# Kernel tuning notes

Measured on AMD Instinct MI355X. Metric: run time of the kernel, lower is better.

Reference implementation:

```python
import jax, jax.numpy as jnp
import numpy as np

N_NODES = 102400
N_EDGES = 1638400
N_REL = 8
D_IN = 256


def setup_inputs() -> dict:
    key = jax.random.key(0)
    ks = jax.random.split(key, 8)
    b_z = jax.random.normal(ks[0], (N_NODES, D_IN), dtype=jnp.float32)
    b_edge_index = jax.random.randint(ks[1], (2, N_EDGES), 0, N_NODES, dtype=jnp.int64)
    b_edge_weights = jax.random.uniform(ks[2], (N_EDGES,), dtype=jnp.float32)
    b_edge_types = jax.random.randint(ks[3], (N_EDGES,), 0, N_REL, dtype=jnp.int64)
    # Glorot-ish init scaled by fan-in
    W1 = jax.random.normal(ks[4], (N_REL, 256, 128), dtype=jnp.float32) / np.sqrt(256.0)
    W2 = jax.random.normal(ks[5], (N_REL, 128, 64), dtype=jnp.float32) / np.sqrt(128.0)
    W3 = jax.random.normal(ks[6], (N_REL, 64, 1), dtype=jnp.float32) / np.sqrt(64.0)
    return {
        "b_z": b_z,
        "b_edge_index": b_edge_index,
        "b_edge_weights": b_edge_weights,
        "b_edge_types": b_edge_types,
        "W1": W1, "bias1": jnp.zeros((128,), jnp.float32),
        "W2": W2, "bias2": jnp.zeros((64,), jnp.float32),
        "W3": W3, "bias3": jnp.zeros((1,), jnp.float32),
        "b_size": 512,
    }


def rgcn_conv(x, src, dst, etype, ew, W, b):
    """Relation-specific transform + weighted scatter-add (root_weight=False).

    x: [N, d_in], W: [R, d_in, d_out], b: [d_out]
    """
    n = x.shape[0]
    # Transform node features under every relation: [R, N, d_out]
    xw = jnp.einsum('nd,rdo->rno', x, W)
    # Per-edge message = W_{etype[e]} @ x[src[e]], scaled by edge weight
    msgs = xw[etype, src] * ew[:, None]          # [E, d_out]
    out = jax.ops.segment_sum(msgs, dst, num_segments=n)  # scatter-add at targets
    return out + b


def reference(b_z, b_edge_index, b_edge_weights, b_edge_types,
              W1, bias1, W2, bias2, W3, bias3, b_size):
    src, dst = b_edge_index[0], b_edge_index[1]
    h = rgcn_conv(b_z, src, dst, b_edge_types, b_edge_weights, W1, bias1)
    h = jax.nn.relu(h)
    h = rgcn_conv(h, src, dst, b_edge_types, b_edge_weights, W2, bias2)
    h = jax.nn.relu(h)
    h = rgcn_conv(h, src, dst, b_edge_types, b_edge_weights, W3, bias3)  # [N, 1]
    x_hat = h.reshape(b_size, -1)
    return x_hat
```

## Files before the change

kernel.cpp:

```cpp
#include <hip/hip_runtime.h>
#include <hip/hip_bf16.h>
#include <hip/hip_fp16.h>
#include <cstdint>

#define N_NODES 102400
#define N_EDGES 1638400
#define N_REL   8
#define D0      256
#define D1      128
#define D2      64

#define WIN     256
#define NBIN    (N_NODES / WIN)
#define CHA     8192
#define NBLKA   (N_EDGES / CHA)

typedef __attribute__((ext_vector_type(8))) short          s16x8;
typedef __attribute__((ext_vector_type(8))) unsigned short u16x8;
typedef __attribute__((ext_vector_type(4))) float          f32x4;

__device__ __forceinline__ unsigned short f2bf(float f) {
    unsigned u = __float_as_uint(f);
    u += 0x7fffu + ((u >> 16) & 1u);
    return (unsigned short)(u >> 16);
}
__device__ __forceinline__ float h2f_bits(unsigned short u) {
    __half_raw r; r.x = u;
    return __half2float(__half(r));
}

__global__ __launch_bounds__(256) void fill0_k(int* __restrict__ p, int total) {
    int i = blockIdx.x * 256 + threadIdx.x;
    if (i < total) p[i] = 0;
}

__global__ __launch_bounds__(256) void countA_k(const int* __restrict__ dst,
                                                int* __restrict__ bincnt) {
    __shared__ int h[NBIN];
    const int t  = threadIdx.x;
    const int e0 = blockIdx.x * CHA;
    for (int i = t; i < NBIN; i += 256) h[i] = 0;
    __syncthreads();
#pragma unroll
    for (int i = 0; i < CHA / 256; ++i) {
        int e = e0 + t + i * 256;
        if (e < N_EDGES) atomicAdd(&h[dst[e] >> 8], 1);
    }
    __syncthreads();
    for (int i = t; i < NBIN; i += 256) {
        int c = h[i];
        if (c) atomicAdd(&bincnt[i], c);
    }
}

__device__ __forceinline__ int block_scan_excl_512(int v, int* sA, int* sB, int t) {
    sA[t] = v;
    __syncthreads();
    int* s = sA; int* d = sB;
    for (int o = 1; o < 512; o <<= 1) {
        int x = s[t];
        if (t >= o) x += s[t - o];
        d[t] = x;
        __syncthreads();
        int* tmp = s; s = d; d = tmp;
    }
    return s[t] - v;
}

__global__ __launch_bounds__(512) void scanB_k(const int* __restrict__ bincnt,
                                               int* __restrict__ binbase,
                                               int* __restrict__ bincur) {
    __shared__ int sA[512], sB[512];
    const int t = threadIdx.x;
    int v = (t < NBIN) ? bincnt[t] : 0;
    int excl = block_scan_excl_512(v, sA, sB, t);
    if (t < NBIN) { binbase[t] = excl; bincur[t] = excl; }
    if (t == 0) binbase[NBIN] = N_EDGES;
}

__global__ __launch_bounds__(256) void scatterA_k(const int* __restrict__ src,
                                                  const int* __restrict__ dst,
                                                  const float* __restrict__ ew,
                                                  const int* __restrict__ et,
                                                  int* __restrict__ bincur,
                                                  uint2* __restrict__ temp) {
    __shared__ int h[NBIN];
    const int t  = threadIdx.x;
    const int e0 = blockIdx.x * CHA;
    for (int i = t; i < NBIN; i += 256) h[i] = 0;
    __syncthreads();
#pragma unroll
    for (int i = 0; i < CHA / 256; ++i) {
        int e = e0 + t + i * 256;
        if (e < N_EDGES) atomicAdd(&h[dst[e] >> 8], 1);
    }
    __syncthreads();
    for (int i = t; i < NBIN; i += 256) {
        int c = h[i];
        h[i] = c ? atomicAdd(&bincur[i], c) : 0;
    }
    __syncthreads();
#pragma unroll
    for (int i = 0; i < CHA / 256; ++i) {
        int e = e0 + t + i * 256;
        if (e < N_EDGES) {
            int d   = dst[e];
            int bin = d >> 8;
            unsigned hb = (unsigned)(__half_raw(__float2half(ew[e])).x);
            unsigned g  = (unsigned)(et[e] * N_NODES + src[e]);
            int pos = atomicAdd(&h[bin], 1);
            temp[pos] = make_uint2(g, (hb << 8) | (unsigned)(d & 255));
        }
    }
}

__global__ __launch_bounds__(512) void passB_k(const uint2* __restrict__ temp,
                                               const int* __restrict__ binbase,
                                               int* __restrict__ off,
                                               unsigned* __restrict__ eg,
                                               unsigned short* __restrict__ ewh) {
    __shared__ int hist[WIN];
    __shared__ int sA[512], sB[512];
    const int b    = blockIdx.x;
    const int t    = threadIdx.x;
    const int beg  = binbase[b], end = binbase[b + 1];
    const int key0 = b * WIN;
    if (t < WIN) hist[t] = 0;
    __syncthreads();
    for (int j = beg + t; j < end; j += 512)
        atomicAdd(&hist[temp[j].y & 255], 1);
    __syncthreads();
    int v = (t < WIN) ? hist[t] : 0;
    int excl = block_scan_excl_512(v, sA, sB, t) + beg;
    if (t < WIN) {
        off[key0 + t] = excl;
        hist[t] = excl;
    }
    __syncthreads();
    for (int j = beg + t; j < end; j += 512) {
        uint2 e = temp[j];
        int pos = atomicAdd(&hist[e.y & 255], 1);
        eg[pos]  = e.x;
        ewh[pos] = (unsigned short)(e.y >> 8);
    }
    if (b == 0 && t == 0) off[N_NODES] = N_EDGES;
}

__global__ __launch_bounds__(256) void cvt_wT_k(const float* __restrict__ in,
                                                unsigned short* __restrict__ out,
                                                int K, int Nn, int total) {
    int o = blockIdx.x * 256 + threadIdx.x;
    if (o < total) {
        int kn = K * Nn;
        int r = o / kn, rem = o % kn;
        int n = rem / K, k = rem % K;
        out[o] = f2bf(in[r * kn + k * Nn + n]);
    }
}

template<int DIN, int DOUT, bool AF32>
__global__ __launch_bounds__(256) void mfma_gemm_b(const void* __restrict__ Av,
                                                   const unsigned short* __restrict__ Bt0,
                                                   __half* __restrict__ C0) {
    constexpr int BM  = 128;
    constexpr int BK  = 64;
    constexpr int BN  = DOUT;
    constexpr int LDK = BK + 8;
    constexpr int FM  = (BM / 2) / 16;
    constexpr int FN  = (BN / 2) / 16;

    __shared__ __align__(16) unsigned short As[BM][LDK];
    __shared__ __align__(16) unsigned short Bs[BN][LDK];

    const unsigned short* Bt = Bt0 + (size_t)blockIdx.y * DIN * DOUT;
    __half*               C  = C0  + (size_t)blockIdx.y * N_NODES * DOUT;

    const int tid  = threadIdx.x;
    const int wave = tid >> 6;
    const int lane = tid & 63;
    const int lr   = lane & 15;
    const int kq   = lane >> 4;
    const int wm   = (wave >> 1) * (BM / 2);
    const int wn   = (wave & 1) * (BN / 2);
    const int row0 = blockIdx.x * BM;

    f32x4 acc[FM][FN];
#pragma unroll
    for (int i = 0; i < FM; ++i)
#pragma unroll
        for (int j = 0; j < FN; ++j) acc[i][j] = (f32x4){0.f, 0.f, 0.f, 0.f};

    for (int kt = 0; kt < DIN; kt += BK) {
        constexpr int NA = BM * BK / 8;
#pragma unroll
        for (int i = 0; i < NA / 256; ++i) {
            int idx = tid + i * 256;
            int r = idx >> 3;
            int c = (idx & 7) * 8;
            u16x8 v;
            if constexpr (AF32) {
                const float* ap = (const float*)Av + (size_t)(row0 + r) * DIN + kt + c;
                float4 u0 = *reinterpret_cast<const float4*>(ap);
                float4 u1 = *reinterpret_cast<const float4*>(ap + 4);
                v[0] = (short)f2bf(u0.x); v[1] = (short)f2bf(u0.y);
                v[2] = (short)f2bf(u0.z); v[3] = (short)f2bf(u0.w);
                v[4] = (short)f2bf(u1.x); v[5] = (short)f2bf(u1.y);
                v[6] = (short)f2bf(u1.z); v[7] = (short)f2bf(u1.w);
            } else {
                v = *reinterpret_cast<const u16x8*>(
                    (const unsigned short*)Av + (size_t)(row0 + r) * DIN + kt + c);
            }
            *reinterpret_cast<u16x8*>(&As[r][c]) = v;
        }
        constexpr int NB = BN * BK / 8;
#pragma unroll
        for (int i = 0; i < NB / 256; ++i) {
            int idx = tid + i * 256;
            int r = idx >> 3;
            int c = (idx & 7) * 8;
            u16x8 v = *reinterpret_cast<const u16x8*>(&Bt[(size_t)r * DIN + kt + c]);
            *reinterpret_cast<u16x8*>(&Bs[r][c]) = v;
        }
        __syncthreads();

#pragma unroll
        for (int ks = 0; ks < BK; ks += 32) {
            s16x8 af[FM], bfr[FN];
#pragma unroll
            for (int mi = 0; mi < FM; ++mi)
                af[mi] = *reinterpret_cast<const s16x8*>(&As[wm + mi * 16 + lr][ks + kq * 8]);
#pragma unroll
            for (int ni = 0; ni < FN; ++ni)
                bfr[ni] = *reinterpret_cast<const s16x8*>(&Bs[wn + ni * 16 + lr][ks + kq * 8]);
#pragma unroll
            for (int mi = 0; mi < FM; ++mi)
#pragma unroll
                for (int ni = 0; ni < FN; ++ni)
                    acc[mi][ni] = __builtin_amdgcn_mfma_f32_16x16x32_bf16(
                        af[mi], bfr[ni], acc[mi][ni], 0, 0, 0);
        }
        __syncthreads();
    }

#pragma unroll
    for (int mi = 0; mi < FM; ++mi) {
#pragma unroll
        for (int ni = 0; ni < FN; ++ni) {
#pragma unroll
            for (int reg = 0; reg < 4; ++reg) {
                int rrow = row0 + wm + mi * 16 + kq * 4 + reg;
                int ccol = wn + ni * 16 + lr;
                C[(size_t)rrow * DOUT + ccol] = __float2half(acc[mi][ni][reg]);
            }
        }
    }
}

template<int DOUT, bool RELUOUT>
__global__ __launch_bounds__(256) void agg_flat(const int* __restrict__ off,
                                                const unsigned* __restrict__ eg,
                                                const unsigned short* __restrict__ ewh,
                                                const __half* __restrict__ xw,
                                                const float* __restrict__ bias,
                                                float* __restrict__ hf,
                                                unsigned short* __restrict__ hb) {
    const int node = (blockIdx.x * 256 + threadIdx.x) >> 6;
    const int lane = threadIdx.x & 63;
    if (node >= N_NODES) return;
    const int beg = off[node], end = off[node + 1];

    if (DOUT == 128) {
        float ax = bias[lane * 2], ay = bias[lane * 2 + 1];
        int j = beg;
        for (; j + 4 <= end; j += 4) {
            unsigned g0 = eg[j], g1 = eg[j + 1], g2 = eg[j + 2], g3 = eg[j + 3];
            float w0 = h2f_bits(ewh[j]),     w1 = h2f_bits(ewh[j + 1]);
            float w2 = h2f_bits(ewh[j + 2]), w3 = h2f_bits(ewh[j + 3]);
            __half2 v0 = *reinterpret_cast<const __half2*>(&xw[(size_t)g0 * 128 + lane * 2]);
            __half2 v1 = *reinterpret_cast<const __half2*>(&xw[(size_t)g1 * 128 + lane * 2]);
            __half2 v2 = *reinterpret_cast<const __half2*>(&xw[(size_t)g2 * 128 + lane * 2]);
            __half2 v3 = *reinterpret_cast<const __half2*>(&xw[(size_t)g3 * 128 + lane * 2]);
            float2 f0 = __half22float2(v0), f1 = __half22float2(v1);
            float2 f2 = __half22float2(v2), f3 = __half22float2(v3);
            ax += w0 * f0.x + w1 * f1.x + w2 * f2.x + w3 * f3.x;
            ay += w0 * f0.y + w1 * f1.y + w2 * f2.y + w3 * f3.y;
        }
        for (; j < end; ++j) {
            unsigned g = eg[j];
            float    w = h2f_bits(ewh[j]);
            __half2  v = *reinterpret_cast<const __half2*>(&xw[(size_t)g * 128 + lane * 2]);
            float2   f = __half22float2(v);
            ax += w * f.x;
            ay += w * f.y;
        }
        if (RELUOUT) {
            unsigned pk = (unsigned)f2bf(fmaxf(ax, 0.f)) |
                          ((unsigned)f2bf(fmaxf(ay, 0.f)) << 16);
            *reinterpret_cast<unsigned*>(&hb[(size_t)node * 128 + lane * 2]) = pk;
        } else {
            *reinterpret_cast<float2*>(&hf[(size_t)node * 128 + lane * 2]) =
                make_float2(ax, ay);
        }
    } else {
        float a = bias[lane];
        int j = beg;
        for (; j + 4 <= end; j += 4) {
            unsigned g0 = eg[j], g1 = eg[j + 1], g2 = eg[j + 2], g3 = eg[j + 3];
            float w0 = h2f_bits(ewh[j]),     w1 = h2f_bits(ewh[j + 1]);
            float w2 = h2f_bits(ewh[j + 2]), w3 = h2f_bits(ewh[j + 3]);
            float f0 = __half2float(xw[(size_t)g0 * 64 + lane]);
            float f1 = __half2float(xw[(size_t)g1 * 64 + lane]);
            float f2 = __half2float(xw[(size_t)g2 * 64 + lane]);
            float f3 = __half2float(xw[(size_t)g3 * 64 + lane]);
            a += w0 * f0 + w1 * f1 + w2 * f2 + w3 * f3;
        }
        for (; j < end; ++j)
            a += h2f_bits(ewh[j]) * __half2float(xw[(size_t)eg[j] * 64 + lane]);
        hf[(size_t)node * 64 + lane] = a;
    }
}

__global__ __launch_bounds__(256) void xw3_kernel(const float* __restrict__ h2,
                                                  const float* __restrict__ W3,
                                                  float* __restrict__ xw3) {
    __shared__ float w[D2];
    const int r = blockIdx.y;
    for (int i = threadIdx.x; i < D2; i += 256) w[i] = W3[r * D2 + i];
    __syncthreads();
    int n = blockIdx.x * 256 + threadIdx.x;
    if (n < N_NODES) {
        const float4* hp = reinterpret_cast<const float4*>(h2 + (size_t)n * D2);
        float s = 0.f;
#pragma unroll
        for (int d4 = 0; d4 < D2 / 4; ++d4) {
            float4 v = hp[d4];
            s += fmaxf(v.x, 0.f) * w[d4 * 4]     + fmaxf(v.y, 0.f) * w[d4 * 4 + 1] +
                 fmaxf(v.z, 0.f) * w[d4 * 4 + 2] + fmaxf(v.w, 0.f) * w[d4 * 4 + 3];
        }
        xw3[(size_t)r * N_NODES + n] = s;
    }
}

__global__ __launch_bounds__(256) void final_k(const int* __restrict__ off,
                                               const unsigned* __restrict__ eg,
                                               const unsigned short* __restrict__ ewh,
                                               const float* __restrict__ xw3,
                                               const float* __restrict__ b3,
                                               float* __restrict__ out) {
    int d = blockIdx.x * 256 + threadIdx.x;
    if (d >= N_NODES) return;
    float acc = b3[0];
    const int beg = off[d], end = off[d + 1];
    int j = beg;
    for (; j + 4 <= end; j += 4) {
        float w0 = h2f_bits(ewh[j]),     w1 = h2f_bits(ewh[j + 1]);
        float w2 = h2f_bits(ewh[j + 2]), w3 = h2f_bits(ewh[j + 3]);
        float x0 = xw3[eg[j]],     x1 = xw3[eg[j + 1]];
        float x2 = xw3[eg[j + 2]], x3 = xw3[eg[j + 3]];
        acc += w0 * x0 + w1 * x1 + w2 * x2 + w3 * x3;
    }
    for (; j < end; ++j)
        acc += h2f_bits(ewh[j]) * xw3[eg[j]];
    out[d] = acc;
}

extern "C" void kernel_launch(void* const* d_in, const int* in_sizes, int n_in,
                              void* d_out, int out_size, void* d_ws, size_t ws_size,
                              hipStream_t stream) {
    (void)in_sizes; (void)n_in; (void)out_size; (void)ws_size;

    const float* z    = (const float*)d_in[0];
    const int*   eidx = (const int*)d_in[1];
    const float* ew   = (const float*)d_in[2];
    const int*   et   = (const int*)d_in[3];
    const float* W1   = (const float*)d_in[4];
    const float* b1   = (const float*)d_in[5];
    const float* W2   = (const float*)d_in[6];
    const float* b2   = (const float*)d_in[7];
    const float* W3   = (const float*)d_in[8];
    const float* b3   = (const float*)d_in[9];

    const int* src = eidx;
    const int* dst = eidx + N_EDGES;

    char* ws = (char*)d_ws;
    size_t o = 0;
    auto alloc = [&](size_t bytes) { char* p = ws + o; o += (bytes + 255) & ~(size_t)255; return p; };
    int*      off     = (int*)     alloc((size_t)(N_NODES + 1) * 4);
    int*      bincnt  = (int*)     alloc((size_t)NBIN * 4);
    int*      binbase = (int*)     alloc((size_t)(NBIN + 1) * 4);
    int*      bincur  = (int*)     alloc((size_t)NBIN * 4);
    unsigned* eg      = (unsigned*)alloc((size_t)N_EDGES * 4);
    unsigned short* ewh = (unsigned short*)alloc((size_t)N_EDGES * 2);
    unsigned short* Wt1 = (unsigned short*)alloc((size_t)N_REL * D0 * D1 * 2);
    unsigned short* Wt2 = (unsigned short*)alloc((size_t)N_REL * D1 * D2 * 2);
    char*     UNION   =            alloc((size_t)N_NODES * D1 * 2);
    __half*   xw_all  = (__half*)  alloc((size_t)N_REL * N_NODES * D1 * 2);

    uint2*          temp = (uint2*)UNION;
    unsigned short* h1b  = (unsigned short*)UNION;
    __half*         xw2  = xw_all;
    float*          h2f  = (float*)((char*)xw_all + (size_t)N_REL * N_NODES * D2 * 2);
    float*          xw3f = (float*)xw_all;
    float* out = (float*)d_out;

    fill0_k<<<(NBIN + 255) / 256, 256, 0, stream>>>(bincnt, NBIN);
    countA_k<<<NBLKA, 256, 0, stream>>>(dst, bincnt);
    scanB_k<<<1, 512, 0, stream>>>(bincnt, binbase, bincur);
    scatterA_k<<<NBLKA, 256, 0, stream>>>(src, dst, ew, et, bincur, temp);
    passB_k<<<NBIN, 512, 0, stream>>>(temp, binbase, off, eg, ewh);

    cvt_wT_k<<<(N_REL * D0 * D1 + 255) / 256, 256, 0, stream>>>(W1, Wt1, D0, D1, N_REL * D0 * D1);
    cvt_wT_k<<<(N_REL * D1 * D2 + 255) / 256, 256, 0, stream>>>(W2, Wt2, D1, D2, N_REL * D1 * D2);

    constexpr int AGG_BLKS = N_NODES / 4;

    mfma_gemm_b<D0, D1, true><<<dim3(N_NODES / 128, N_REL), 256, 0, stream>>>(
        z, Wt1, xw_all);
    agg_flat<D1, true><<<AGG_BLKS, 256, 0, stream>>>(off, eg, ewh, xw_all, b1, nullptr, h1b);

    mfma_gemm_b<D1, D2, false><<<dim3(N_NODES / 128, N_REL), 256, 0, stream>>>(
        h1b, Wt2, xw2);
    agg_flat<D2, false><<<AGG_BLKS, 256, 0, stream>>>(off, eg, ewh, xw2, b2, h2f, nullptr);

    xw3_kernel<<<dim3((N_NODES + 255) / 256, N_REL), 256, 0, stream>>>(h2f, W3, xw3f);
    final_k<<<(N_NODES + 255) / 256, 256, 0, stream>>>(off, eg, ewh, xw3f, b3, out);
}
```

Baseline: 655.6 us.

## Split layer-1 aggregation across two waves per node and pre-convert z to bf16

Layer-1 aggregation now gives each node two wavefronts, each covering 64 of the 128 output dims with scalar half loads, which doubles wave-level parallelism for the gather but halves the bytes per load. When the workspace is large enough, z is first converted to bf16 in a separate pass so the first GEMM reads bf16 instead of fp32 with in-kernel conversion. The conversion pass adds an extra read and write of z, and the workspace layout now depends on the available size.

```diff
diff --git a/kernel.cpp b/kernel.cpp
--- a/kernel.cpp
+++ b/kernel.cpp
@@ -144,6 +144,18 @@
         ewh[pos] = (unsigned short)(e.y >> 8);
     }
     if (b == 0 && t == 0) off[N_NODES] = N_EDGES;
+}
+
+__global__ __launch_bounds__(256) void cvt_bf16_k(const float* __restrict__ in,
+                                                  unsigned short* __restrict__ out,
+                                                  int n4) {
+    int i = blockIdx.x * 256 + threadIdx.x;
+    if (i < n4) {
+        float4 v = reinterpret_cast<const float4*>(in)[i];
+        ushort4 o;
+        o.x = f2bf(v.x); o.y = f2bf(v.y); o.z = f2bf(v.z); o.w = f2bf(v.w);
+        reinterpret_cast<ushort4*>(out)[i] = o;
+    }
 }
 
 __global__ __launch_bounds__(256) void cvt_wT_k(const float* __restrict__ in,
@@ -264,44 +276,37 @@
                                                 const float* __restrict__ bias,
                                                 float* __restrict__ hf,
                                                 unsigned short* __restrict__ hb) {
-    const int node = (blockIdx.x * 256 + threadIdx.x) >> 6;
-    const int lane = threadIdx.x & 63;
-    if (node >= N_NODES) return;
-    const int beg = off[node], end = off[node + 1];
+    const int gwave = (blockIdx.x * 256 + threadIdx.x) >> 6;
+    const int lane  = threadIdx.x & 63;
 
     if (DOUT == 128) {
-        float ax = bias[lane * 2], ay = bias[lane * 2 + 1];
+        const int node = gwave >> 1;
+        const int dim  = (gwave & 1) * 64 + lane;
+        if (node >= N_NODES) return;
+        const int beg = off[node], end = off[node + 1];
+        float a = bias[dim];
         int j = beg;
         for (; j + 4 <= end; j += 4) {
             unsigned g0 = eg[j], g1 = eg[j + 1], g2 = eg[j + 2], g3 = eg[j + 3];
             float w0 = h2f_bits(ewh[j]),     w1 = h2f_bits(ewh[j + 1]);
             float w2 = h2f_bits(ewh[j + 2]), w3 = h2f_bits(ewh[j + 3]);
-            __half2 v0 = *reinterpret_cast<const __half2*>(&xw[(size_t)g0 * 128 + lane * 2]);
-            __half2 v1 = *reinterpret_cast<const __half2*>(&xw[(size_t)g1 * 128 + lane * 2]);
-            __half2 v2 = *reinterpret_cast<const __half2*>(&xw[(size_t)g2 * 128 + lane * 2]);
-            __half2 v3 = *reinterpret_cast<const __half2*>(&xw[(size_t)g3 * 128 + lane * 2]);
-            float2 f0 = __half22float2(v0), f1 = __half22float2(v1);
-            float2 f2 = __half22float2(v2), f3 = __half22float2(v3);
-            ax += w0 * f0.x + w1 * f1.x + w2 * f2.x + w3 * f3.x;
-            ay += w0 * f0.y + w1 * f1.y + w2 * f2.y + w3 * f3.y;
-        }
-        for (; j < end; ++j) {
-            unsigned g = eg[j];
-            float    w = h2f_bits(ewh[j]);
-            __half2  v = *reinterpret_cast<const __half2*>(&xw[(size_t)g * 128 + lane * 2]);
-            float2   f = __half22float2(v);
-            ax += w * f.x;
-            ay += w * f.y;
-        }
+            float f0 = __half2float(xw[(size_t)g0 * 128 + dim]);
+            float f1 = __half2float(xw[(size_t)g1 * 128 + dim]);
+            float f2 = __half2float(xw[(size_t)g2 * 128 + dim]);
+            float f3 = __half2float(xw[(size_t)g3 * 128 + dim]);
+            a += w0 * f0 + w1 * f1 + w2 * f2 + w3 * f3;
+        }
+        for (; j < end; ++j)
+            a += h2f_bits(ewh[j]) * __half2float(xw[(size_t)eg[j] * 128 + dim]);
         if (RELUOUT) {
-            unsigned pk = (unsigned)f2bf(fmaxf(ax, 0.f)) |
-                          ((unsigned)f2bf(fmaxf(ay, 0.f)) << 16);
-            *reinterpret_cast<unsigned*>(&hb[(size_t)node * 128 + lane * 2]) = pk;
+            hb[(size_t)node * 128 + dim] = f2bf(fmaxf(a, 0.f));
         } else {
-            *reinterpret_cast<float2*>(&hf[(size_t)node * 128 + lane * 2]) =
-                make_float2(ax, ay);
+            hf[(size_t)node * 128 + dim] = a;
         }
     } else {
+        const int node = gwave;
+        if (node >= N_NODES) return;
+        const int beg = off[node], end = off[node + 1];
         float a = bias[lane];
         int j = beg;
         for (; j + 4 <= end; j += 4) {
@@ -367,7 +372,7 @@
 extern "C" void kernel_launch(void* const* d_in, const int* in_sizes, int n_in,
                               void* d_out, int out_size, void* d_ws, size_t ws_size,
                               hipStream_t stream) {
-    (void)in_sizes; (void)n_in; (void)out_size; (void)ws_size;
+    (void)in_sizes; (void)n_in; (void)out_size;
 
     const float* z    = (const float*)d_in[0];
     const int*   eidx = (const int*)d_in[1];
@@ -382,6 +387,17 @@
 
     const int* src = eidx;
     const int* dst = eidx + N_EDGES;
+
+    auto pad = [](size_t b) { return (b + 255) & ~(size_t)255; };
+    const size_t sz_small  = pad((size_t)N_NODES * D1 * 2);
+    const size_t sz_big    = pad((size_t)N_NODES * D0 * 2);
+    const size_t sz_common =
+        pad((size_t)(N_NODES + 1) * 4) + pad((size_t)NBIN * 4) +
+        pad((size_t)(NBIN + 1) * 4) + pad((size_t)NBIN * 4) +
+        pad((size_t)N_EDGES * 4) + pad((size_t)N_EDGES * 2) +
+        pad((size_t)N_REL * D0 * D1 * 2) + pad((size_t)N_REL * D1 * D2 * 2) +
+        pad((size_t)N_REL * N_NODES * D1 * 2);
+    const bool big = ws_size >= sz_common + sz_big + (1u << 20);
 
     char* ws = (char*)d_ws;
     size_t o = 0;
@@ -394,10 +410,11 @@
     unsigned short* ewh = (unsigned short*)alloc((size_t)N_EDGES * 2);
     unsigned short* Wt1 = (unsigned short*)alloc((size_t)N_REL * D0 * D1 * 2);
     unsigned short* Wt2 = (unsigned short*)alloc((size_t)N_REL * D1 * D2 * 2);
-    char*     UNION   =            alloc((size_t)N_NODES * D1 * 2);
+    char*     UNION   =            alloc(big ? sz_big : sz_small);
     __half*   xw_all  = (__half*)  alloc((size_t)N_REL * N_NODES * D1 * 2);
 
     uint2*          temp = (uint2*)UNION;
+    unsigned short* z_bf = (unsigned short*)UNION;
     unsigned short* h1b  = (unsigned short*)UNION;
     __half*         xw2  = xw_all;
     float*          h2f  = (float*)((char*)xw_all + (size_t)N_REL * N_NODES * D2 * 2);
@@ -413,15 +430,20 @@
     cvt_wT_k<<<(N_REL * D0 * D1 + 255) / 256, 256, 0, stream>>>(W1, Wt1, D0, D1, N_REL * D0 * D1);
     cvt_wT_k<<<(N_REL * D1 * D2 + 255) / 256, 256, 0, stream>>>(W2, Wt2, D1, D2, N_REL * D1 * D2);
 
-    constexpr int AGG_BLKS = N_NODES / 4;
-
-    mfma_gemm_b<D0, D1, true><<<dim3(N_NODES / 128, N_REL), 256, 0, stream>>>(
-        z, Wt1, xw_all);
-    agg_flat<D1, true><<<AGG_BLKS, 256, 0, stream>>>(off, eg, ewh, xw_all, b1, nullptr, h1b);
+    if (big) {
+        cvt_bf16_k<<<(N_NODES * D0 / 4 + 255) / 256, 256, 0, stream>>>(
+            z, z_bf, N_NODES * D0 / 4);
+        mfma_gemm_b<D0, D1, false><<<dim3(N_NODES / 128, N_REL), 256, 0, stream>>>(
+            z_bf, Wt1, xw_all);
+    } else {
+        mfma_gemm_b<D0, D1, true><<<dim3(N_NODES / 128, N_REL), 256, 0, stream>>>(
+            z, Wt1, xw_all);
+    }
+    agg_flat<D1, true><<<N_NODES / 2, 256, 0, stream>>>(off, eg, ewh, xw_all, b1, nullptr, h1b);
 
     mfma_gemm_b<D1, D2, false><<<dim3(N_NODES / 128, N_REL), 256, 0, stream>>>(
         h1b, Wt2, xw2);
-    agg_flat<D2, false><<<AGG_BLKS, 256, 0, stream>>>(off, eg, ewh, xw2, b2, h2f, nullptr);
+    agg_flat<D2, false><<<N_NODES / 4, 256, 0, stream>>>(off, eg, ewh, xw2, b2, h2f, nullptr);
 
     xw3_kernel<<<dim3((N_NODES + 255) / 256, N_REL), 256, 0, stream>>>(h2f, W3, xw3f);
     final_k<<<(N_NODES + 255) / 256, 256, 0, stream>>>(off, eg, ewh, xw3f, b3, out);
```

After: 702.9 us. 7.2% more time.
